# Kernel optimization log

Measured on AMD Instinct MI355X. Metric: run time of the kernel, lower is better.

The kernel has to match this reference:

```python
import jax, jax.numpy as jnp
import numpy as np

B, N, HID, HEADS = 4, 512, 64, 4
D = HID // HEADS          # head_dim = 16
E_DIM = 1
SCALE = 1.0 / np.sqrt(D)
LN_EPS = 1e-5
NEG = -1e9


def _linear_init(k, fan_in, fan_out):
    lim = 1.0 / np.sqrt(fan_in)
    kw, kb = jax.random.split(k)
    W = jax.random.uniform(kw, (fan_in, fan_out), jnp.float32, -lim, lim)
    b = jax.random.uniform(kb, (fan_out,), jnp.float32, -lim, lim)
    return W, b


def setup_inputs() -> dict:
    key = jax.random.key(0)
    ks = jax.random.split(key, 8)
    W1_w, W1_b = _linear_init(ks[3], HID, HID)
    W2_w, W2_b = _linear_init(ks[4], HID, HID)
    W3_w, W3_b = _linear_init(ks[5], HID, HID)
    W4_w, W4_b = _linear_init(ks[6], HID, HID)
    W5_w, W5_b = _linear_init(ks[7], E_DIM, HID)
    return {
        "x": jax.random.normal(ks[0], (B, N, HID), jnp.float32),
        "adj": jax.random.randint(ks[1], (B, N, N), 0, 2, jnp.int32),
        "edge_features": jax.random.normal(ks[2], (B, N, N, E_DIM), jnp.float32),
        "W1_w": W1_w, "W1_b": W1_b,
        "W2_w": W2_w, "W2_b": W2_b,
        "W3_w": W3_w, "W3_b": W3_b,
        "W4_w": W4_w, "W4_b": W4_b,
        "W5_w": W5_w, "W5_b": W5_b,
        "ln_g": jnp.ones((HID,), jnp.float32),
        "ln_b": jnp.zeros((HID,), jnp.float32),
    }


def _layer_norm(y, g, b):
    m = jnp.mean(y, axis=-1, keepdims=True)
    v = jnp.mean(jnp.square(y - m), axis=-1, keepdims=True)
    return (y - m) * jax.lax.rsqrt(v + LN_EPS) * g + b


def reference(x, adj, edge_features, W1_w, W1_b, W2_w, W2_b, W3_w, W3_b,
              W4_w, W4_b, W5_w, W5_b, ln_g, ln_b):
    b, n, h = x.shape
    self_t = x @ W1_w + W1_b                               # [B,N,HID]
    Q = (x @ W3_w + W3_b).reshape(b, n, HEADS, D)          # [B,N,H,D]
    K = (x @ W4_w + W4_b).reshape(b, n, HEADS, D)          # [B,N,H,D]
    # edge contribution: W5 e_ij -> [B,N,N,H,D] (the big intermediate)
    Ec = (edge_features @ W5_w + W5_b).reshape(b, n, n, HEADS, D)
    # (Q_i . (K_j + E_ij)) split into node-pair GEMM + edge broadcast term
    scores = (jnp.einsum('bihd,bjhd->bhij', Q, K)
              + jnp.einsum('bihd,bijhd->bhij', Q, Ec)) * SCALE  # [B,H,N,N]
    scores = jnp.where(adj[:, None, :, :] == 0, NEG, scores)
    attn = jax.nn.softmax(scores, axis=-1)                 # dropout = identity (eval)
    V = (x @ W2_w + W2_b).reshape(b, n, HEADS, D)          # [B,N,H,D]
    msg = jnp.einsum('bhij,bjhd->bihd', attn, V).reshape(b, n, h)
    return _layer_norm(x + self_t + msg, ln_g, ln_b)
```

## Files before the change

### kernel.cpp

```cpp
#include <hip/hip_runtime.h>

#define B 4
#define N 512
#define HID 64
#define HEADS 4
#define DH 16
#define SCALE 0.25f
#define LN_EPS 1e-5f

constexpr int ROWS = B * N;
constexpr size_t OFF_ST  = 0;
constexpr size_t OFF_Q   = (size_t)ROWS * HID;
constexpr size_t OFF_K   = 2 * OFF_Q;
constexpr size_t OFF_V   = 3 * OFF_Q;
constexpr size_t OFF_PART= 4 * OFF_Q;

__global__ __launch_bounds__(256) void proj_kernel(
    const float* __restrict__ x,
    const float* __restrict__ W1w, const float* __restrict__ W1b,
    const float* __restrict__ W2w, const float* __restrict__ W2b,
    const float* __restrict__ W3w, const float* __restrict__ W3b,
    const float* __restrict__ W4w, const float* __restrict__ W4b,
    float* __restrict__ ws)
{
  __shared__ float xsT[64 * 4];
  const int t = threadIdx.x;
  const int rows0 = blockIdx.x * 4;

  if (t < 64) {
    const float4 v = *(const float4*)&x[(size_t)rows0 * HID + t * 4];
    const int r = t >> 4;
    const int k0 = (t & 15) * 4;
    xsT[(k0 + 0) * 4 + r] = v.x;
    xsT[(k0 + 1) * 4 + r] = v.y;
    xsT[(k0 + 2) * 4 + r] = v.z;
    xsT[(k0 + 3) * 4 + r] = v.w;
  }
  __syncthreads();

  const int m = t >> 6;
  const int c = t & 63;
  const float* Ww; const float* Wb; size_t off;
  if      (m == 0) { Ww = W1w; Wb = W1b; off = OFF_ST; }
  else if (m == 1) { Ww = W3w; Wb = W3b; off = OFF_Q;  }
  else if (m == 2) { Ww = W4w; Wb = W4b; off = OFF_K;  }
  else             { Ww = W2w; Wb = W2b; off = OFF_V;  }

  float acc[4];
#pragma unroll
  for (int r = 0; r < 4; ++r) acc[r] = 0.f;

#pragma unroll 16
  for (int k = 0; k < 64; ++k) {
    const float w = Ww[(k << 6) + c];
    const float4 a0 = *(const float4*)&xsT[k * 4];
    acc[0] = fmaf(a0.x, w, acc[0]); acc[1] = fmaf(a0.y, w, acc[1]);
    acc[2] = fmaf(a0.z, w, acc[2]); acc[3] = fmaf(a0.w, w, acc[3]);
  }

  const float bias = Wb[c];
  const size_t base = off + (size_t)rows0 * HID + c;
#pragma unroll
  for (int r = 0; r < 4; ++r)
    ws[base + (size_t)r * HID] = acc[r] + bias;
}

__global__ __launch_bounds__(256, 4) void attn_kernel(
    const int*   __restrict__ adj,
    const float* __restrict__ efeat,
    const float* __restrict__ W5w, const float* __restrict__ W5b,
    float* __restrict__ ws)
{
  __shared__ float KV[512 * 20];

  const int it = blockIdx.x, h = blockIdx.y;
  const int b  = blockIdx.z >> 2;
  const int qt = blockIdx.z & 3;
  const int j0 = qt << 7;
  const int t = threadIdx.x;
  const int g  = t & 15;
  const int il = t >> 4;
  const int iA = it * 32 + il;
  const int iB = iA + 16;

  const float* Qb = ws + OFF_Q;
  const float* Kb = ws + OFF_K;
  const float* Vb = ws + OFF_V;
  float* part = ws + OFF_PART;

  float* Ksh = KV;
  float* Vsh = KV + 2560;

  {
    const int sj = t >> 2;
    const int dq = (t & 3) << 2;
#pragma unroll
    for (int p = 0; p < 2; ++p) {
      const int j  = sj + (p << 6);
      const int sr = ((j & 3) << 5) | (j >> 2);
      const size_t gb = ((size_t)(b * N + j0 + j)) * HID + h * DH + dq;
      *(float4*)&Ksh[sr * 20 + dq] = *(const float4*)&Kb[gb];
      *(float4*)&Vsh[sr * 20 + dq] = *(const float4*)&Vb[gb];
    }
  }

  const float4 w50 = *(const float4*)&W5w[h * DH];
  const float4 w51 = *(const float4*)&W5w[h * DH + 4];
  const float4 w52 = *(const float4*)&W5w[h * DH + 8];
  const float4 w53 = *(const float4*)&W5w[h * DH + 12];
  const float4 b50 = *(const float4*)&W5b[h * DH];
  const float4 b51 = *(const float4*)&W5b[h * DH + 4];
  const float4 b52 = *(const float4*)&W5b[h * DH + 8];
  const float4 b53 = *(const float4*)&W5b[h * DH + 12];

  float4 qA0, qA1, qA2, qA3, qB0, qB1, qB2, qB3;
  float qw5A, qb5A, qw5B, qb5B;
  {
    const float* qr = Qb + ((size_t)(b * N + iA)) * HID + h * DH;
    qA0 = *(const float4*)(qr);     qA1 = *(const float4*)(qr + 4);
    qA2 = *(const float4*)(qr + 8); qA3 = *(const float4*)(qr + 12);
    qw5A = qA0.x*w50.x + qA0.y*w50.y + qA0.z*w50.z + qA0.w*w50.w
         + qA1.x*w51.x + qA1.y*w51.y + qA1.z*w51.z + qA1.w*w51.w
         + qA2.x*w52.x + qA2.y*w52.y + qA2.z*w52.z + qA2.w*w52.w
         + qA3.x*w53.x + qA3.y*w53.y + qA3.z*w53.z + qA3.w*w53.w;
    qb5A = qA0.x*b50.x + qA0.y*b50.y + qA0.z*b50.z + qA0.w*b50.w
         + qA1.x*b51.x + qA1.y*b51.y + qA1.z*b51.z + qA1.w*b51.w
         + qA2.x*b52.x + qA2.y*b52.y + qA2.z*b52.z + qA2.w*b52.w
         + qA3.x*b53.x + qA3.y*b53.y + qA3.z*b53.z + qA3.w*b53.w;
  }
  {
    const float* qr = Qb + ((size_t)(b * N + iB)) * HID + h * DH;
    qB0 = *(const float4*)(qr);     qB1 = *(const float4*)(qr + 4);
    qB2 = *(const float4*)(qr + 8); qB3 = *(const float4*)(qr + 12);
    qw5B = qB0.x*w50.x + qB0.y*w50.y + qB0.z*w50.z + qB0.w*w50.w
         + qB1.x*w51.x + qB1.y*w51.y + qB1.z*w51.z + qB1.w*w51.w
         + qB2.x*w52.x + qB2.y*w52.y + qB2.z*w52.z + qB2.w*w52.w
         + qB3.x*w53.x + qB3.y*w53.y + qB3.z*w53.z + qB3.w*w53.w;
    qb5B = qB0.x*b50.x + qB0.y*b50.y + qB0.z*b50.z + qB0.w*b50.w
         + qB1.x*b51.x + qB1.y*b51.y + qB1.z*b51.z + qB1.w*b51.w
         + qB2.x*b52.x + qB2.y*b52.y + qB2.z*b52.z + qB2.w*b52.w
         + qB3.x*b53.x + qB3.y*b53.y + qB3.z*b53.z + qB3.w*b53.w;
  }

  float cA[8], cB[8];
  {
    const int*   aR = adj   + ((size_t)(b * N + iA)) * N + j0;
    const float* eR = efeat + ((size_t)(b * N + iA)) * N + j0;
    const int4   a0 = *(const int4*)&aR[4 * g];
    const int4   a1 = *(const int4*)&aR[4 * g + 64];
    const float4 e0 = *(const float4*)&eR[4 * g];
    const float4 e1 = *(const float4*)&eR[4 * g + 64];
    cA[0] = a0.x ? SCALE * fmaf(e0.x, qw5A, qb5A) : -1e9f;
    cA[1] = a0.y ? SCALE * fmaf(e0.y, qw5A, qb5A) : -1e9f;
    cA[2] = a0.z ? SCALE * fmaf(e0.z, qw5A, qb5A) : -1e9f;
    cA[3] = a0.w ? SCALE * fmaf(e0.w, qw5A, qb5A) : -1e9f;
    cA[4] = a1.x ? SCALE * fmaf(e1.x, qw5A, qb5A) : -1e9f;
    cA[5] = a1.y ? SCALE * fmaf(e1.y, qw5A, qb5A) : -1e9f;
    cA[6] = a1.z ? SCALE * fmaf(e1.z, qw5A, qb5A) : -1e9f;
    cA[7] = a1.w ? SCALE * fmaf(e1.w, qw5A, qb5A) : -1e9f;
  }
  {
    const int*   aR = adj   + ((size_t)(b * N + iB)) * N + j0;
    const float* eR = efeat + ((size_t)(b * N + iB)) * N + j0;
    const int4   a0 = *(const int4*)&aR[4 * g];
    const int4   a1 = *(const int4*)&aR[4 * g + 64];
    const float4 e0 = *(const float4*)&eR[4 * g];
    const float4 e1 = *(const float4*)&eR[4 * g + 64];
    cB[0] = a0.x ? SCALE * fmaf(e0.x, qw5B, qb5B) : -1e9f;
    cB[1] = a0.y ? SCALE * fmaf(e0.y, qw5B, qb5B) : -1e9f;
    cB[2] = a0.z ? SCALE * fmaf(e0.z, qw5B, qb5B) : -1e9f;
    cB[3] = a0.w ? SCALE * fmaf(e0.w, qw5B, qb5B) : -1e9f;
    cB[4] = a1.x ? SCALE * fmaf(e1.x, qw5B, qb5B) : -1e9f;
    cB[5] = a1.y ? SCALE * fmaf(e1.y, qw5B, qb5B) : -1e9f;
    cB[6] = a1.z ? SCALE * fmaf(e1.z, qw5B, qb5B) : -1e9f;
    cB[7] = a1.w ? SCALE * fmaf(e1.w, qw5B, qb5B) : -1e9f;
  }

  __syncthreads();

  float lA = 0.f, lB = 0.f;
  float accA[16], accB[16];
#pragma unroll
  for (int d = 0; d < 16; ++d) { accA[d] = 0.f; accB[d] = 0.f; }

#pragma unroll
  for (int q = 0; q < 2; ++q) {
#pragma unroll
    for (int r = 0; r < 4; ++r) {
      const int idx = (q << 2) | r;
      const int sr = (r << 5) | (g + (q << 4));
      const float* kr = &Ksh[sr * 20];
      const float4 k0 = *(const float4*)(kr);
      const float4 k1 = *(const float4*)(kr + 4);
      const float4 k2 = *(const float4*)(kr + 8);
      const float4 k3 = *(const float4*)(kr + 12);
      float a0 = qA0.x*k0.x + qA0.y*k0.y + qA0.z*k0.z + qA0.w*k0.w;
      a0 = fmaf(qA1.x,k1.x, fmaf(qA1.y,k1.y, fmaf(qA1.z,k1.z, fmaf(qA1.w,k1.w, a0))));
      a0 = fmaf(qA2.x,k2.x, fmaf(qA2.y,k2.y, fmaf(qA2.z,k2.z, fmaf(qA2.w,k2.w, a0))));
      a0 = fmaf(qA3.x,k3.x, fmaf(qA3.y,k3.y, fmaf(qA3.z,k3.z, fmaf(qA3.w,k3.w, a0))));
      float b0 = qB0.x*k0.x + qB0.y*k0.y + qB0.z*k0.z + qB0.w*k0.w;
      b0 = fmaf(qB1.x,k1.x, fmaf(qB1.y,k1.y, fmaf(qB1.z,k1.z, fmaf(qB1.w,k1.w, b0))));
      b0 = fmaf(qB2.x,k2.x, fmaf(qB2.y,k2.y, fmaf(qB2.z,k2.z, fmaf(qB2.w,k2.w, b0))));
      b0 = fmaf(qB3.x,k3.x, fmaf(qB3.y,k3.y, fmaf(qB3.z,k3.z, fmaf(qB3.w,k3.w, b0))));

      const float pA = __expf(fmaf(a0, SCALE, cA[idx]));
      const float pB = __expf(fmaf(b0, SCALE, cB[idx]));
      lA += pA; lB += pB;

      const float* vr = &Vsh[sr * 20];
      const float4 v0 = *(const float4*)(vr);
      const float4 v1 = *(const float4*)(vr + 4);
      const float4 v2 = *(const float4*)(vr + 8);
      const float4 v3 = *(const float4*)(vr + 12);
      accA[0] = fmaf(pA,v0.x,accA[0]); accA[1] = fmaf(pA,v0.y,accA[1]);
      accA[2] = fmaf(pA,v0.z,accA[2]); accA[3] = fmaf(pA,v0.w,accA[3]);
      accA[4] = fmaf(pA,v1.x,accA[4]); accA[5] = fmaf(pA,v1.y,accA[5]);
      accA[6] = fmaf(pA,v1.z,accA[6]); accA[7] = fmaf(pA,v1.w,accA[7]);
      accA[8] = fmaf(pA,v2.x,accA[8]); accA[9] = fmaf(pA,v2.y,accA[9]);
      accA[10]= fmaf(pA,v2.z,accA[10]);accA[11]= fmaf(pA,v2.w,accA[11]);
      accA[12]= fmaf(pA,v3.x,accA[12]);accA[13]= fmaf(pA,v3.y,accA[13]);
      accA[14]= fmaf(pA,v3.z,accA[14]);accA[15]= fmaf(pA,v3.w,accA[15]);
      accB[0] = fmaf(pB,v0.x,accB[0]); accB[1] = fmaf(pB,v0.y,accB[1]);
      accB[2] = fmaf(pB,v0.z,accB[2]); accB[3] = fmaf(pB,v0.w,accB[3]);
      accB[4] = fmaf(pB,v1.x,accB[4]); accB[5] = fmaf(pB,v1.y,accB[5]);
      accB[6] = fmaf(pB,v1.z,accB[6]); accB[7] = fmaf(pB,v1.w,accB[7]);
      accB[8] = fmaf(pB,v2.x,accB[8]); accB[9] = fmaf(pB,v2.y,accB[9]);
      accB[10]= fmaf(pB,v2.z,accB[10]);accB[11]= fmaf(pB,v2.w,accB[11]);
      accB[12]= fmaf(pB,v3.x,accB[12]);accB[13]= fmaf(pB,v3.y,accB[13]);
      accB[14]= fmaf(pB,v3.z,accB[14]);accB[15]= fmaf(pB,v3.w,accB[15]);
    }
  }

#pragma unroll
  for (int o = 1; o < 16; o <<= 1) {
    lA += __shfl_xor(lA, o, 16);
    lB += __shfl_xor(lB, o, 16);
  }

  __syncthreads();
  float* P = KV;
  const int baseA = (il * 16 + g) * 20;
  const int baseB = ((il + 16) * 16 + g) * 20;
  *(float4*)&P[baseA+ 0] = make_float4(accA[0],  accA[1],  accA[2],  accA[3]);
  *(float4*)&P[baseA+ 4] = make_float4(accA[4],  accA[5],  accA[6],  accA[7]);
  *(float4*)&P[baseA+ 8] = make_float4(accA[8],  accA[9],  accA[10], accA[11]);
  *(float4*)&P[baseA+12] = make_float4(accA[12], accA[13], accA[14], accA[15]);
  *(float4*)&P[baseB+ 0] = make_float4(accB[0],  accB[1],  accB[2],  accB[3]);
  *(float4*)&P[baseB+ 4] = make_float4(accB[4],  accB[5],  accB[6],  accB[7]);
  *(float4*)&P[baseB+ 8] = make_float4(accB[8],  accB[9],  accB[10], accB[11]);
  *(float4*)&P[baseB+12] = make_float4(accB[12], accB[13], accB[14], accB[15]);
  __syncthreads();

  float sumA = 0.f, sumB = 0.f;
#pragma unroll
  for (int gp = 0; gp < 16; ++gp) {
    sumA += P[(il * 16 + gp) * 20 + g];
    sumB += P[((il + 16) * 16 + gp) * 20 + g];
  }

  float* recA = part + ((((size_t)(b * N + iA)) * HEADS + h) * 4 + qt) * 20;
  float* recB = part + ((((size_t)(b * N + iB)) * HEADS + h) * 4 + qt) * 20;
  recA[g] = sumA;
  recB[g] = sumB;
  if (g == 0) { recA[16] = lA; recB[16] = lB; }
}

__global__ __launch_bounds__(256) void ln_kernel(
    const float* __restrict__ x, const float* __restrict__ ws,
    const float* __restrict__ gamma, const float* __restrict__ beta,
    float* __restrict__ out)
{
  const int t = threadIdx.x;
  const int lane = t & 63;
  const int row = blockIdx.x * 4 + (t >> 6);
  const size_t idx = (size_t)row * HID + lane;
  const float* ST   = ws + OFF_ST;
  const float* part = ws + OFF_PART;

  const int h = lane >> 4;
  const int d = lane & 15;
  const float* rec = part + (((size_t)row * HEADS + h) * 4) * 20;
  const float num = rec[d] + rec[20 + d] + rec[40 + d] + rec[60 + d];
  const float den = rec[16] + rec[20 + 16] + rec[40 + 16] + rec[60 + 16];
  const float msg = num / den;

  const float v = x[idx] + ST[idx] + msg;
  float mu = v;
#pragma unroll
  for (int o = 1; o < 64; o <<= 1) mu += __shfl_xor(mu, o, 64);
  mu *= (1.0f / 64.0f);
  const float dv = v - mu;
  float var = dv * dv;
#pragma unroll
  for (int o = 1; o < 64; o <<= 1) var += __shfl_xor(var, o, 64);
  var *= (1.0f / 64.0f);
  out[idx] = dv * rsqrtf(var + LN_EPS) * gamma[lane] + beta[lane];
}

extern "C" void kernel_launch(void* const* d_in, const int* in_sizes, int n_in,
                              void* d_out, int out_size, void* d_ws, size_t ws_size,
                              hipStream_t stream)
{
  const float* x   = (const float*)d_in[0];
  const int*   adj = (const int*)d_in[1];
  const float* ef  = (const float*)d_in[2];
  const float* W1w = (const float*)d_in[3];
  const float* W1b = (const float*)d_in[4];
  const float* W2w = (const float*)d_in[5];
  const float* W2b = (const float*)d_in[6];
  const float* W3w = (const float*)d_in[7];
  const float* W3b = (const float*)d_in[8];
  const float* W4w = (const float*)d_in[9];
  const float* W4b = (const float*)d_in[10];
  const float* W5w = (const float*)d_in[11];
  const float* W5b = (const float*)d_in[12];
  const float* lng = (const float*)d_in[13];
  const float* lnb = (const float*)d_in[14];
  float* ws  = (float*)d_ws;
  float* out = (float*)d_out;

  proj_kernel<<<ROWS / 4, 256, 0, stream>>>(x, W1w, W1b, W2w, W2b, W3w, W3b, W4w, W4b, ws);
  attn_kernel<<<dim3(16, HEADS, B * 4), 256, 0, stream>>>(adj, ef, W5w, W5b, ws);
  ln_kernel<<<ROWS / 4, 256, 0, stream>>>(x, ws, lng, lnb, out);
}
```

Baseline: 22.29 us.

## Store Q/K/V in fp16 and use packed half2 math in attention

The projection kernel now writes Q, K and V as fp16 into the workspace, while self_t stays fp32. The attention kernel stages K/V in shared memory as half with a 24-element row stride, and computes the QK dot products and PV accumulation with packed __hfma2. The aim is to halve global and LDS traffic for K/V and roughly halve the ALU instruction count in the inner loop. In exchange, softmax weights and the value accumulation run in fp16, which costs accuracy and could exceed tolerance.

```diff
diff --git a/kernel.cpp b/kernel.cpp
--- a/kernel.cpp
+++ b/kernel.cpp
@@ -1,4 +1,5 @@
 #include <hip/hip_runtime.h>
+#include <hip/hip_fp16.h>
 
 #define B 4
 #define N 512
@@ -14,6 +15,8 @@
 constexpr size_t OFF_K   = 2 * OFF_Q;
 constexpr size_t OFF_V   = 3 * OFF_Q;
 constexpr size_t OFF_PART= 4 * OFF_Q;
+
+struct H8 { __half2 h[4]; };
 
 __global__ __launch_bounds__(256) void proj_kernel(
     const float* __restrict__ x,
@@ -59,10 +62,18 @@
   }
 
   const float bias = Wb[c];
-  const size_t base = off + (size_t)rows0 * HID + c;
-#pragma unroll
-  for (int r = 0; r < 4; ++r)
-    ws[base + (size_t)r * HID] = acc[r] + bias;
+  if (m == 0) {
+    const size_t base = (size_t)rows0 * HID + c;
+#pragma unroll
+    for (int r = 0; r < 4; ++r)
+      ws[base + (size_t)r * HID] = acc[r] + bias;
+  } else {
+    __half* hd = (__half*)(ws + off);
+    const size_t base = (size_t)rows0 * HID + c;
+#pragma unroll
+    for (int r = 0; r < 4; ++r)
+      hd[base + (size_t)r * HID] = __float2half_rn(acc[r] + bias);
+  }
 }
 
 __global__ __launch_bounds__(256, 4) void attn_kernel(
@@ -72,6 +83,8 @@
     float* __restrict__ ws)
 {
   __shared__ float KV[512 * 20];
+  __half* Ksh = (__half*)KV;
+  __half* Vsh = ((__half*)KV) + 3072;
 
   const int it = blockIdx.x, h = blockIdx.y;
   const int b  = blockIdx.z >> 2;
@@ -83,63 +96,52 @@
   const int iA = it * 32 + il;
   const int iB = iA + 16;
 
-  const float* Qb = ws + OFF_Q;
-  const float* Kb = ws + OFF_K;
-  const float* Vb = ws + OFF_V;
+  const __half* Qh = (const __half*)(ws + OFF_Q);
+  const __half* Kh = (const __half*)(ws + OFF_K);
+  const __half* Vh = (const __half*)(ws + OFF_V);
   float* part = ws + OFF_PART;
 
-  float* Ksh = KV;
-  float* Vsh = KV + 2560;
-
-  {
-    const int sj = t >> 2;
-    const int dq = (t & 3) << 2;
-#pragma unroll
-    for (int p = 0; p < 2; ++p) {
-      const int j  = sj + (p << 6);
-      const int sr = ((j & 3) << 5) | (j >> 2);
-      const size_t gb = ((size_t)(b * N + j0 + j)) * HID + h * DH + dq;
-      *(float4*)&Ksh[sr * 20 + dq] = *(const float4*)&Kb[gb];
-      *(float4*)&Vsh[sr * 20 + dq] = *(const float4*)&Vb[gb];
-    }
-  }
-
-  const float4 w50 = *(const float4*)&W5w[h * DH];
-  const float4 w51 = *(const float4*)&W5w[h * DH + 4];
-  const float4 w52 = *(const float4*)&W5w[h * DH + 8];
-  const float4 w53 = *(const float4*)&W5w[h * DH + 12];
-  const float4 b50 = *(const float4*)&W5b[h * DH];
-  const float4 b51 = *(const float4*)&W5b[h * DH + 4];
-  const float4 b52 = *(const float4*)&W5b[h * DH + 8];
-  const float4 b53 = *(const float4*)&W5b[h * DH + 12];
-
-  float4 qA0, qA1, qA2, qA3, qB0, qB1, qB2, qB3;
-  float qw5A, qb5A, qw5B, qb5B;
-  {
-    const float* qr = Qb + ((size_t)(b * N + iA)) * HID + h * DH;
-    qA0 = *(const float4*)(qr);     qA1 = *(const float4*)(qr + 4);
-    qA2 = *(const float4*)(qr + 8); qA3 = *(const float4*)(qr + 12);
-    qw5A = qA0.x*w50.x + qA0.y*w50.y + qA0.z*w50.z + qA0.w*w50.w
-         + qA1.x*w51.x + qA1.y*w51.y + qA1.z*w51.z + qA1.w*w51.w
-         + qA2.x*w52.x + qA2.y*w52.y + qA2.z*w52.z + qA2.w*w52.w
-         + qA3.x*w53.x + qA3.y*w53.y + qA3.z*w53.z + qA3.w*w53.w;
-    qb5A = qA0.x*b50.x + qA0.y*b50.y + qA0.z*b50.z + qA0.w*b50.w
-         + qA1.x*b51.x + qA1.y*b51.y + qA1.z*b51.z + qA1.w*b51.w
-         + qA2.x*b52.x + qA2.y*b52.y + qA2.z*b52.z + qA2.w*b52.w
-         + qA3.x*b53.x + qA3.y*b53.y + qA3.z*b53.z + qA3.w*b53.w;
-  }
-  {
-    const float* qr = Qb + ((size_t)(b * N + iB)) * HID + h * DH;
-    qB0 = *(const float4*)(qr);     qB1 = *(const float4*)(qr + 4);
-    qB2 = *(const float4*)(qr + 8); qB3 = *(const float4*)(qr + 12);
-    qw5B = qB0.x*w50.x + qB0.y*w50.y + qB0.z*w50.z + qB0.w*w50.w
-         + qB1.x*w51.x + qB1.y*w51.y + qB1.z*w51.z + qB1.w*w51.w
-         + qB2.x*w52.x + qB2.y*w52.y + qB2.z*w52.z + qB2.w*w52.w
-         + qB3.x*w53.x + qB3.y*w53.y + qB3.z*w53.z + qB3.w*w53.w;
-    qb5B = qB0.x*b50.x + qB0.y*b50.y + qB0.z*b50.z + qB0.w*b50.w
-         + qB1.x*b51.x + qB1.y*b51.y + qB1.z*b51.z + qB1.w*b51.w
-         + qB2.x*b52.x + qB2.y*b52.y + qB2.z*b52.z + qB2.w*b52.w
-         + qB3.x*b53.x + qB3.y*b53.y + qB3.z*b53.z + qB3.w*b53.w;
+  {
+    const int j  = t >> 1;
+    const int pr = t & 1;
+    const int sr = ((j & 3) << 5) | (j >> 2);
+    const size_t gb = ((size_t)(b * N + j0 + j)) * HID + h * DH + pr * 8;
+    *(float4*)&Ksh[sr * 24 + pr * 8] = *(const float4*)&Kh[gb];
+    *(float4*)&Vsh[sr * 24 + pr * 8] = *(const float4*)&Vh[gb];
+  }
+
+  __half2 qA2[8], qB2[8];
+  {
+    const size_t qb = ((size_t)(b * N + iA)) * HID + h * DH;
+    H8 q0 = *reinterpret_cast<const H8*>(&Qh[qb]);
+    H8 q1 = *reinterpret_cast<const H8*>(&Qh[qb + 8]);
+#pragma unroll
+    for (int k = 0; k < 4; ++k) { qA2[k] = q0.h[k]; qA2[k + 4] = q1.h[k]; }
+  }
+  {
+    const size_t qb = ((size_t)(b * N + iB)) * HID + h * DH;
+    H8 q0 = *reinterpret_cast<const H8*>(&Qh[qb]);
+    H8 q1 = *reinterpret_cast<const H8*>(&Qh[qb + 8]);
+#pragma unroll
+    for (int k = 0; k < 4; ++k) { qB2[k] = q0.h[k]; qB2[k + 4] = q1.h[k]; }
+  }
+
+  float qAf[16], qBf[16];
+#pragma unroll
+  for (int k = 0; k < 8; ++k) {
+    const float2 fa = __half22float2(qA2[k]);
+    const float2 fb = __half22float2(qB2[k]);
+    qAf[2 * k] = fa.x; qAf[2 * k + 1] = fa.y;
+    qBf[2 * k] = fb.x; qBf[2 * k + 1] = fb.y;
+  }
+
+  float qw5A = 0.f, qb5A = 0.f, qw5B = 0.f, qb5B = 0.f;
+#pragma unroll
+  for (int k = 0; k < 16; ++k) {
+    const float w5 = W5w[h * DH + k];
+    const float b5 = W5b[h * DH + k];
+    qw5A = fmaf(qAf[k], w5, qw5A); qb5A = fmaf(qAf[k], b5, qb5A);
+    qw5B = fmaf(qBf[k], w5, qw5B); qb5B = fmaf(qBf[k], b5, qb5B);
   }
 
   float cA[8], cB[8];
@@ -179,9 +181,12 @@
   __syncthreads();
 
   float lA = 0.f, lB = 0.f;
-  float accA[16], accB[16];
-#pragma unroll
-  for (int d = 0; d < 16; ++d) { accA[d] = 0.f; accB[d] = 0.f; }
+  __half2 accA2[8], accB2[8];
+#pragma unroll
+  for (int k = 0; k < 8; ++k) {
+    accA2[k] = __float2half2_rn(0.f);
+    accB2[k] = __float2half2_rn(0.f);
+  }
 
 #pragma unroll
   for (int q = 0; q < 2; ++q) {
@@ -189,45 +194,39 @@
     for (int r = 0; r < 4; ++r) {
       const int idx = (q << 2) | r;
       const int sr = (r << 5) | (g + (q << 4));
-      const float* kr = &Ksh[sr * 20];
-      const float4 k0 = *(const float4*)(kr);
-      const float4 k1 = *(const float4*)(kr + 4);
-      const float4 k2 = *(const float4*)(kr + 8);
-      const float4 k3 = *(const float4*)(kr + 12);
-      float a0 = qA0.x*k0.x + qA0.y*k0.y + qA0.z*k0.z + qA0.w*k0.w;
-      a0 = fmaf(qA1.x,k1.x, fmaf(qA1.y,k1.y, fmaf(qA1.z,k1.z, fmaf(qA1.w,k1.w, a0))));
-      a0 = fmaf(qA2.x,k2.x, fmaf(qA2.y,k2.y, fmaf(qA2.z,k2.z, fmaf(qA2.w,k2.w, a0))));
-      a0 = fmaf(qA3.x,k3.x, fmaf(qA3.y,k3.y, fmaf(qA3.z,k3.z, fmaf(qA3.w,k3.w, a0))));
-      float b0 = qB0.x*k0.x + qB0.y*k0.y + qB0.z*k0.z + qB0.w*k0.w;
-      b0 = fmaf(qB1.x,k1.x, fmaf(qB1.y,k1.y, fmaf(qB1.z,k1.z, fmaf(qB1.w,k1.w, b0))));
-      b0 = fmaf(qB2.x,k2.x, fmaf(qB2.y,k2.y, fmaf(qB2.z,k2.z, fmaf(qB2.w,k2.w, b0))));
-      b0 = fmaf(qB3.x,k3.x, fmaf(qB3.y,k3.y, fmaf(qB3.z,k3.z, fmaf(qB3.w,k3.w, b0))));
-
-      const float pA = __expf(fmaf(a0, SCALE, cA[idx]));
-      const float pB = __expf(fmaf(b0, SCALE, cB[idx]));
+      const __half* kr = &Ksh[sr * 24];
+      const H8 k0 = *reinterpret_cast<const H8*>(kr);
+      const H8 k1 = *reinterpret_cast<const H8*>(kr + 8);
+
+      __half2 dA = __hmul2(qA2[0], k0.h[0]);
+      __half2 dB = __hmul2(qB2[0], k0.h[0]);
+      dA = __hfma2(qA2[1], k0.h[1], dA); dB = __hfma2(qB2[1], k0.h[1], dB);
+      dA = __hfma2(qA2[2], k0.h[2], dA); dB = __hfma2(qB2[2], k0.h[2], dB);
+      dA = __hfma2(qA2[3], k0.h[3], dA); dB = __hfma2(qB2[3], k0.h[3], dB);
+      dA = __hfma2(qA2[4], k1.h[0], dA); dB = __hfma2(qB2[4], k1.h[0], dB);
+      dA = __hfma2(qA2[5], k1.h[1], dA); dB = __hfma2(qB2[5], k1.h[1], dB);
+      dA = __hfma2(qA2[6], k1.h[2], dA); dB = __hfma2(qB2[6], k1.h[2], dB);
+      dA = __hfma2(qA2[7], k1.h[3], dA); dB = __hfma2(qB2[7], k1.h[3], dB);
+      const float sA = __low2float(dA) + __high2float(dA);
+      const float sB = __low2float(dB) + __high2float(dB);
+
+      const float pA = __expf(fmaf(sA, SCALE, cA[idx]));
+      const float pB = __expf(fmaf(sB, SCALE, cB[idx]));
       lA += pA; lB += pB;
-
-      const float* vr = &Vsh[sr * 20];
-      const float4 v0 = *(const float4*)(vr);
-      const float4 v1 = *(const float4*)(vr + 4);
-      const float4 v2 = *(const float4*)(vr + 8);
-      const float4 v3 = *(const float4*)(vr + 12);
-      accA[0] = fmaf(pA,v0.x,accA[0]); accA[1] = fmaf(pA,v0.y,accA[1]);
-      accA[2] = fmaf(pA,v0.z,accA[2]); accA[3] = fmaf(pA,v0.w,accA[3]);
-      accA[4] = fmaf(pA,v1.x,accA[4]); accA[5] = fmaf(pA,v1.y,accA[5]);
-      accA[6] = fmaf(pA,v1.z,accA[6]); accA[7] = fmaf(pA,v1.w,accA[7]);
-      accA[8] = fmaf(pA,v2.x,accA[8]); accA[9] = fmaf(pA,v2.y,accA[9]);
-      accA[10]= fmaf(pA,v2.z,accA[10]);accA[11]= fmaf(pA,v2.w,accA[11]);
-      accA[12]= fmaf(pA,v3.x,accA[12]);accA[13]= fmaf(pA,v3.y,accA[13]);
-      accA[14]= fmaf(pA,v3.z,accA[14]);accA[15]= fmaf(pA,v3.w,accA[15]);
-      accB[0] = fmaf(pB,v0.x,accB[0]); accB[1] = fmaf(pB,v0.y,accB[1]);
-      accB[2] = fmaf(pB,v0.z,accB[2]); accB[3] = fmaf(pB,v0.w,accB[3]);
-      accB[4] = fmaf(pB,v1.x,accB[4]); accB[5] = fmaf(pB,v1.y,accB[5]);
-      accB[6] = fmaf(pB,v1.z,accB[6]); accB[7] = fmaf(pB,v1.w,accB[7]);
-      accB[8] = fmaf(pB,v2.x,accB[8]); accB[9] = fmaf(pB,v2.y,accB[9]);
-      accB[10]= fmaf(pB,v2.z,accB[10]);accB[11]= fmaf(pB,v2.w,accB[11]);
-      accB[12]= fmaf(pB,v3.x,accB[12]);accB[13]= fmaf(pB,v3.y,accB[13]);
-      accB[14]= fmaf(pB,v3.z,accB[14]);accB[15]= fmaf(pB,v3.w,accB[15]);
+      const __half2 pA2 = __float2half2_rn(pA);
+      const __half2 pB2 = __float2half2_rn(pB);
+
+      const __half* vr = &Vsh[sr * 24];
+      const H8 v0 = *reinterpret_cast<const H8*>(vr);
+      const H8 v1 = *reinterpret_cast<const H8*>(vr + 8);
+      accA2[0] = __hfma2(pA2, v0.h[0], accA2[0]); accB2[0] = __hfma2(pB2, v0.h[0], accB2[0]);
+      accA2[1] = __hfma2(pA2, v0.h[1], accA2[1]); accB2[1] = __hfma2(pB2, v0.h[1], accB2[1]);
+      accA2[2] = __hfma2(pA2, v0.h[2], accA2[2]); accB2[2] = __hfma2(pB2, v0.h[2], accB2[2]);
+      accA2[3] = __hfma2(pA2, v0.h[3], accA2[3]); accB2[3] = __hfma2(pB2, v0.h[3], accB2[3]);
+      accA2[4] = __hfma2(pA2, v1.h[0], accA2[4]); accB2[4] = __hfma2(pB2, v1.h[0], accB2[4]);
+      accA2[5] = __hfma2(pA2, v1.h[1], accA2[5]); accB2[5] = __hfma2(pB2, v1.h[1], accB2[5]);
+      accA2[6] = __hfma2(pA2, v1.h[2], accA2[6]); accB2[6] = __hfma2(pB2, v1.h[2], accB2[6]);
+      accA2[7] = __hfma2(pA2, v1.h[3], accA2[7]); accB2[7] = __hfma2(pB2, v1.h[3], accB2[7]);
     }
   }
 
@@ -235,6 +234,15 @@
   for (int o = 1; o < 16; o <<= 1) {
     lA += __shfl_xor(lA, o, 16);
     lB += __shfl_xor(lB, o, 16);
+  }
+
+  float accA[16], accB[16];
+#pragma unroll
+  for (int k = 0; k < 8; ++k) {
+    const float2 fa = __half22float2(accA2[k]);
+    const float2 fb = __half22float2(accB2[k]);
+    accA[2 * k] = fa.x; accA[2 * k + 1] = fa.y;
+    accB[2 * k] = fb.x; accB[2 * k + 1] = fb.y;
   }
 
   __syncthreads();
```

Result: no change. 22.01 us (-1.3%).
